# Kernel tuning notes

Measured on AMD Instinct MI355X. Metric: run time of the kernel, lower is better.

Reference implementation:

```python
import jax, jax.numpy as jnp
import numpy as np

NUM_HEADS = 16


def setup_inputs() -> dict:
    k0 = jax.random.key(0)
    ks = jax.random.split(k0, 5)
    T, S, N, E = 1024, 1024, 8, 1024
    query = jax.random.normal(ks[0], (T, N, E), dtype=jnp.float32)
    key_t = jax.random.normal(ks[1], (S, N, E), dtype=jnp.float32)
    value = jax.random.normal(ks[2], (S, N, E), dtype=jnp.float32)
    # xavier-uniform-like scale for in_proj (fan_in=fan_out-ish): gain*sqrt(6/(3E+E))
    lim_in = float(np.sqrt(6.0 / (3 * E + E)))
    in_proj_weight = jax.random.uniform(ks[3], (3 * E, E), dtype=jnp.float32, minval=-lim_in, maxval=lim_in)
    in_proj_bias = jnp.zeros((3 * E,), dtype=jnp.float32)
    lim_out = float(np.sqrt(1.0 / E))
    out_proj_weight = jax.random.uniform(ks[4], (E, E), dtype=jnp.float32, minval=-lim_out, maxval=lim_out)
    out_proj_bias = jnp.zeros((E,), dtype=jnp.float32)
    return {
        'query': query, 'key': key_t, 'value': value,
        'in_proj_weight': in_proj_weight, 'in_proj_bias': in_proj_bias,
        'out_proj_weight': out_proj_weight, 'out_proj_bias': out_proj_bias,
    }


def reference(query, key, value, in_proj_weight, in_proj_bias, out_proj_weight, out_proj_bias):
    # Faithful to the source: q,k,v ALL come from `query` via the 3E in-projection
    # (the torch code projects only `query` and chunks; key/value tensors unused).
    T, N, E = query.shape
    S = key.shape[0]  # must equal T for the reshape, as in the torch code
    H = NUM_HEADS
    D = E // H
    qkv = jnp.einsum('tne,fe->tnf', query, in_proj_weight) + in_proj_bias  # (T,N,3E)
    q, k, v = jnp.split(qkv, 3, axis=-1)
    q = q * (float(D) ** -0.5)
    # (T, N*H, D) -> (N*H, T, D)
    q = q.reshape(T, N * H, D).transpose(1, 0, 2)
    k = k.reshape(S, N * H, D).transpose(1, 0, 2)
    v = v.reshape(S, N * H, D).transpose(1, 0, 2)
    attn = jnp.einsum('btd,bsd->bts', q, k)          # (N*H, T, S)
    attn = jax.nn.softmax(attn, axis=-1)
    out = jnp.einsum('bts,bsd->btd', attn, v)        # (N*H, T, D)
    out = out.transpose(1, 0, 2).reshape(T, N, E)
    out = jnp.einsum('tne,fe->tnf', out, out_proj_weight) + out_proj_bias
    avg_weights = attn.reshape(N, H, T, S).mean(axis=1)  # (N, T, S)
    return out, avg_weights
```

## Files before the change

kernel.cpp:

```cpp
#include <hip/hip_runtime.h>


typedef __bf16 bf16x8 __attribute__((ext_vector_type(8)));
typedef float f32x4 __attribute__((ext_vector_type(4)));
typedef unsigned int u32;
typedef const __attribute__((address_space(1))) u32 gu32;
typedef __attribute__((address_space(3))) u32 lu32;

#define MFMA(a, b, c) __builtin_amdgcn_mfma_f32_16x16x32_bf16((a), (b), (c), 0, 0, 0)

#if __has_builtin(__builtin_amdgcn_exp2f)
#define EXP2(x) __builtin_amdgcn_exp2f(x)
#else
#define EXP2(x) exp2f(x)
#endif

__device__ __forceinline__ unsigned short f2bf(float x) {
    union { float f; unsigned u; } v; v.f = x;
    unsigned r = v.u + 0x7fffu + ((v.u >> 16) & 1u);
    return (unsigned short)(r >> 16);
}

__device__ __forceinline__ bf16x8 frag_ld(const unsigned short* p) {
    return __builtin_bit_cast(bf16x8, *(const uint4*)p);
}

template<int ROWS>
__device__ __forceinline__ void stageNx64(const unsigned short* g, int gs,
                                          unsigned short* lds, int wave, int lane) {
#pragma unroll
    for (int it = 0; it < ROWS / 32; it++) {
        int chunk = wave * (ROWS / 32) + it;
        int row = chunk * 8 + (lane >> 3);
        int cb = (lane & 7) ^ (row & 7);
        const unsigned short* gp = g + (size_t)row * gs + cb * 8;
        unsigned short* lp = lds + chunk * 512;
        __builtin_amdgcn_global_load_lds((gu32*)gp, (lu32*)lp, 16, 0, 0);
    }
}

__device__ __forceinline__ bf16x8 frag_sw(const unsigned short* lds, int row, int cb) {
    return frag_ld(lds + row * 64 + ((cb ^ (row & 7)) << 3));
}

__global__ void k_convert_all(const float* __restrict__ q, const float* __restrict__ wi,
                              const float* __restrict__ wo,
                              unsigned short* __restrict__ xq, unsigned short* __restrict__ xwi,
                              unsigned short* __restrict__ xwo) {
    int i = blockIdx.x * 256 + threadIdx.x;
    const float* src; unsigned short* dst; int off;
    if (i < 2097152)      { src = q;  dst = xq;  off = i; }
    else if (i < 2883584) { src = wi; dst = xwi; off = i - 2097152; }
    else                  { src = wo; dst = xwo; off = i - 2883584; }
    float4 v = ((const float4*)src)[off];
    ushort4 o;
    o.x = f2bf(v.x); o.y = f2bf(v.y); o.z = f2bf(v.z); o.w = f2bf(v.w);
    ((ushort4*)dst)[off] = o;
}

__global__ __launch_bounds__(256) void k_inproj(
    const unsigned short* __restrict__ A, const unsigned short* __restrict__ B,
    const float* __restrict__ bias,
    unsigned short* __restrict__ qbf, unsigned short* __restrict__ kbf,
    unsigned short* __restrict__ vTbf)
{
    __shared__ unsigned short As[2][128 * 64];
    __shared__ unsigned short Bs[2][128 * 64];
    const int tid = threadIdx.x;
    const int wave = tid >> 6, lane = tid & 63;
    const int quad = lane >> 4, l16 = lane & 15;
    const int wm = wave >> 1, wn = wave & 1;
    const int m0 = blockIdx.x * 128, n0 = blockIdx.y * 128;
    const unsigned short* Ab = A + (size_t)m0 * 1024;
    const unsigned short* Bb = B + (size_t)n0 * 1024;

    f32x4 acc[4][4];
#pragma unroll
    for (int i = 0; i < 4; i++)
#pragma unroll
        for (int j = 0; j < 4; j++) acc[i][j] = (f32x4){0.f, 0.f, 0.f, 0.f};

    stageNx64<128>(Ab, 1024, As[0], wave, lane);
    stageNx64<128>(Bb, 1024, Bs[0], wave, lane);
    __syncthreads();
    for (int it = 0; it < 16; it++) {
        const int cur = it & 1;
        if (it < 15) {
            stageNx64<128>(Ab + (it + 1) * 64, 1024, As[cur ^ 1], wave, lane);
            stageNx64<128>(Bb + (it + 1) * 64, 1024, Bs[cur ^ 1], wave, lane);
        }
#pragma unroll
        for (int kc = 0; kc < 2; kc++) {
            bf16x8 af[4], bfr[4];
#pragma unroll
            for (int i = 0; i < 4; i++) af[i]  = frag_sw(As[cur], wm * 64 + i * 16 + l16, kc * 4 + quad);
#pragma unroll
            for (int j = 0; j < 4; j++) bfr[j] = frag_sw(Bs[cur], wn * 64 + j * 16 + l16, kc * 4 + quad);
#pragma unroll
            for (int i = 0; i < 4; i++)
#pragma unroll
                for (int j = 0; j < 4; j++) acc[i][j] = MFMA(af[i], bfr[j], acc[i][j]);
        }
        __syncthreads();
    }
    const float QSCALE = 0.125f * 1.4426950408889634f;
    const int c = n0 >> 10;
#pragma unroll
    for (int i = 0; i < 4; i++) {
#pragma unroll
        for (int j = 0; j < 4; j++) {
            int col = n0 + wn * 64 + j * 16 + l16;
            float bv = bias[col];
            int hd = col & 1023;
#pragma unroll
            for (int r = 0; r < 4; r++) {
                int row = m0 + wm * 64 + i * 16 + quad * 4 + r;
                float val = acc[i][j][r] + bv;
                if (c == 0)      qbf[(size_t)row * 1024 + hd] = f2bf(val * QSCALE);
                else if (c == 1) kbf[(size_t)row * 1024 + hd] = f2bf(val);
                else {
                    int h = hd >> 6, d = hd & 63;
                    int t = row >> 3, n = row & 7;
                    int b = n * 16 + h;
                    vTbf[(size_t)b * 65536 + (size_t)d * 1024 + t] = f2bf(val);
                }
            }
        }
    }
}

__global__ __launch_bounds__(256) void k_pv(
    const unsigned short* __restrict__ qbf, const unsigned short* __restrict__ kbf,
    const unsigned short* __restrict__ vTbf,
    float* __restrict__ il_g, unsigned short* __restrict__ Obf)
{
    __shared__ unsigned short Ks[2][64 * 64];
    __shared__ unsigned short Vs[2][64 * 64];
    __shared__ unsigned short Ps[128 * 64];
    const int tid = threadIdx.x;
    const int wave = tid >> 6, lane = tid & 63, quad = lane >> 4, l16 = lane & 15;
    const int blk = blockIdx.x;
    const int xcd = blk & 7, idx = blk >> 3;
    const int b = xcd * 16 + (idx >> 3);
    const int t0 = (idx & 7) * 128;
    const int n = b >> 4, h = b & 15;
    const size_t vb = (size_t)b * 65536;
    const size_t qkb = (size_t)n * 1024 + h * 64;

    bf16x8 aq[2][2];
#pragma unroll
    for (int rf = 0; rf < 2; rf++)
#pragma unroll
        for (int kh = 0; kh < 2; kh++)
            aq[rf][kh] = frag_ld(&qbf[(size_t)(t0 + wave * 32 + rf * 16 + l16) * 8192 + qkb + kh * 32 + quad * 8]);

    float lsum[2][4];
    f32x4 o[2][4];
#pragma unroll
    for (int rf = 0; rf < 2; rf++)
#pragma unroll
        for (int r = 0; r < 4; r++) lsum[rf][r] = 0.f;
#pragma unroll
    for (int rf = 0; rf < 2; rf++)
#pragma unroll
        for (int df = 0; df < 4; df++) o[rf][df] = (f32x4){0.f, 0.f, 0.f, 0.f};

    stageNx64<64>(kbf + qkb, 8192, Ks[0], wave, lane);
    stageNx64<64>(vTbf + vb, 1024, Vs[0], wave, lane);
    __syncthreads();
    for (int st = 0; st < 16; st++) {
        const int cur = st & 1;
        if (st < 15) {
            stageNx64<64>(kbf + qkb + (size_t)(st + 1) * 524288, 8192, Ks[cur ^ 1], wave, lane);
            stageNx64<64>(vTbf + vb + (st + 1) * 64, 1024, Vs[cur ^ 1], wave, lane);
        }
#pragma unroll
        for (int cf = 0; cf < 4; cf++) {
            bf16x8 k0 = frag_sw(Ks[cur], cf * 16 + l16, quad);
            bf16x8 k1 = frag_sw(Ks[cur], cf * 16 + l16, 4 + quad);
#pragma unroll
            for (int rf = 0; rf < 2; rf++) {
                f32x4 z = (f32x4){0.f, 0.f, 0.f, 0.f};
                z = MFMA(aq[rf][0], k0, z);
                z = MFMA(aq[rf][1], k1, z);
#pragma unroll
                for (int r = 0; r < 4; r++) {
                    float p = EXP2(z[r]);
                    lsum[rf][r] += p;
                    int prow = wave * 32 + rf * 16 + quad * 4 + r;
                    int col = cf * 16 + l16;
                    Ps[prow * 64 + (((col >> 3) ^ (prow & 7)) << 3) + (col & 7)] = f2bf(p);
                }
            }
        }
#pragma unroll
        for (int kc = 0; kc < 2; kc++) {
            bf16x8 ap0 = frag_sw(Ps, wave * 32 + l16, kc * 4 + quad);
            bf16x8 ap1 = frag_sw(Ps, wave * 32 + 16 + l16, kc * 4 + quad);
#pragma unroll
            for (int df = 0; df < 4; df++) {
                bf16x8 bv = frag_sw(Vs[cur], df * 16 + l16, kc * 4 + quad);
                o[0][df] = MFMA(ap0, bv, o[0][df]);
                o[1][df] = MFMA(ap1, bv, o[1][df]);
            }
        }
        __syncthreads();
    }
#pragma unroll
    for (int rf = 0; rf < 2; rf++)
#pragma unroll
        for (int r = 0; r < 4; r++) {
            float s = lsum[rf][r];
            s += __shfl_xor(s, 1); s += __shfl_xor(s, 2);
            s += __shfl_xor(s, 4); s += __shfl_xor(s, 8);
            lsum[rf][r] = 1.0f / s;
        }
#pragma unroll
    for (int rf = 0; rf < 2; rf++)
#pragma unroll
        for (int df = 0; df < 4; df++)
#pragma unroll
            for (int r = 0; r < 4; r++) {
                int t = t0 + wave * 32 + rf * 16 + quad * 4 + r;
                Obf[(size_t)(t * 8 + n) * 1024 + h * 64 + df * 16 + l16] = f2bf(o[rf][df][r] * lsum[rf][r]);
            }
    if (l16 == 0) {
#pragma unroll
        for (int rf = 0; rf < 2; rf++)
#pragma unroll
            for (int r = 0; r < 4; r++)
                il_g[(size_t)b * 1024 + t0 + wave * 32 + rf * 16 + quad * 4 + r] = lsum[rf][r];
    }
}

__global__ __launch_bounds__(256) void k_avg(
    const unsigned short* __restrict__ qbf, const unsigned short* __restrict__ kbf,
    const float* __restrict__ il_g, float* __restrict__ avg)
{
    __shared__ unsigned short Qs[2][128 * 64];
    __shared__ unsigned short Ks[2][128 * 64];
    __shared__ float Is[16 * 128];
    const int tid = threadIdx.x;
    const int wave = tid >> 6, lane = tid & 63, quad = lane >> 4, l16 = lane & 15;
    const int wm = wave >> 1, wn = wave & 1;
    const int blk = blockIdx.x;
    const int n = blk & 7, idx = blk >> 3;
    const int s0 = (idx & 7) * 128, t0 = (idx >> 3) * 128;

    for (int i2 = tid; i2 < 2048; i2 += 256)
        Is[i2] = il_g[(size_t)(n * 16 + (i2 >> 7)) * 1024 + t0 + (i2 & 127)];

    f32x4 acc[4][4];
#pragma unroll
    for (int i = 0; i < 4; i++)
#pragma unroll
        for (int j = 0; j < 4; j++) acc[i][j] = (f32x4){0.f, 0.f, 0.f, 0.f};

    const size_t qb = (size_t)t0 * 8192 + (size_t)n * 1024;
    const size_t kb = (size_t)s0 * 8192 + (size_t)n * 1024;
    stageNx64<128>(qbf + qb, 8192, Qs[0], wave, lane);
    stageNx64<128>(kbf + kb, 8192, Ks[0], wave, lane);
    __syncthreads();
    for (int h = 0; h < 16; h++) {
        const int cur = h & 1;
        if (h < 15) {
            stageNx64<128>(qbf + qb + (h + 1) * 64, 8192, Qs[cur ^ 1], wave, lane);
            stageNx64<128>(kbf + kb + (h + 1) * 64, 8192, Ks[cur ^ 1], wave, lane);
        }
        bf16x8 af[4][2];
        float ir[4][4];
#pragma unroll
        for (int i = 0; i < 4; i++) {
            af[i][0] = frag_sw(Qs[cur], wm * 64 + i * 16 + l16, quad);
            af[i][1] = frag_sw(Qs[cur], wm * 64 + i * 16 + l16, 4 + quad);
#pragma unroll
            for (int r = 0; r < 4; r++) ir[i][r] = Is[h * 128 + wm * 64 + i * 16 + quad * 4 + r];
        }
#pragma unroll
        for (int j = 0; j < 4; j++) {
            bf16x8 b0 = frag_sw(Ks[cur], wn * 64 + j * 16 + l16, quad);
            bf16x8 b1 = frag_sw(Ks[cur], wn * 64 + j * 16 + l16, 4 + quad);
#pragma unroll
            for (int i = 0; i < 4; i++) {
                f32x4 z = (f32x4){0.f, 0.f, 0.f, 0.f};
                z = MFMA(af[i][0], b0, z);
                z = MFMA(af[i][1], b1, z);
#pragma unroll
                for (int r = 0; r < 4; r++)
                    acc[i][j][r] += EXP2(z[r]) * ir[i][r];
            }
        }
        __syncthreads();
    }
#pragma unroll
    for (int i = 0; i < 4; i++)
#pragma unroll
        for (int j = 0; j < 4; j++)
#pragma unroll
            for (int r = 0; r < 4; r++) {
                int t = t0 + wm * 64 + i * 16 + quad * 4 + r;
                int s = s0 + wn * 64 + j * 16 + l16;
                avg[(size_t)n * 1048576 + (size_t)t * 1024 + s] = acc[i][j][r] * 0.0625f;
            }
}

__global__ __launch_bounds__(256) void k_outproj(
    const unsigned short* __restrict__ A, const unsigned short* __restrict__ B,
    const float* __restrict__ bias, float* __restrict__ out)
{
    __shared__ unsigned short As[2][128 * 64];
    __shared__ unsigned short Bs[2][128 * 64];
    const int tid = threadIdx.x;
    const int wave = tid >> 6, lane = tid & 63;
    const int quad = lane >> 4, l16 = lane & 15;
    const int wm = wave >> 1, wn = wave & 1;
    const int m0 = blockIdx.x * 128, n0 = blockIdx.y * 128;
    const unsigned short* Ab = A + (size_t)m0 * 1024;
    const unsigned short* Bb = B + (size_t)n0 * 1024;

    f32x4 acc[4][4];
#pragma unroll
    for (int i = 0; i < 4; i++)
#pragma unroll
        for (int j = 0; j < 4; j++) acc[i][j] = (f32x4){0.f, 0.f, 0.f, 0.f};

    stageNx64<128>(Ab, 1024, As[0], wave, lane);
    stageNx64<128>(Bb, 1024, Bs[0], wave, lane);
    __syncthreads();
    for (int it = 0; it < 16; it++) {
        const int cur = it & 1;
        if (it < 15) {
            stageNx64<128>(Ab + (it + 1) * 64, 1024, As[cur ^ 1], wave, lane);
            stageNx64<128>(Bb + (it + 1) * 64, 1024, Bs[cur ^ 1], wave, lane);
        }
#pragma unroll
        for (int kc = 0; kc < 2; kc++) {
            bf16x8 af[4], bfr[4];
#pragma unroll
            for (int i = 0; i < 4; i++) af[i]  = frag_sw(As[cur], wm * 64 + i * 16 + l16, kc * 4 + quad);
#pragma unroll
            for (int j = 0; j < 4; j++) bfr[j] = frag_sw(Bs[cur], wn * 64 + j * 16 + l16, kc * 4 + quad);
#pragma unroll
            for (int i = 0; i < 4; i++)
#pragma unroll
                for (int j = 0; j < 4; j++) acc[i][j] = MFMA(af[i], bfr[j], acc[i][j]);
        }
        __syncthreads();
    }
#pragma unroll
    for (int i = 0; i < 4; i++)
#pragma unroll
        for (int j = 0; j < 4; j++) {
            int col = n0 + wn * 64 + j * 16 + l16;
            float bv = bias[col];
#pragma unroll
            for (int r = 0; r < 4; r++) {
                int row = m0 + wm * 64 + i * 16 + quad * 4 + r;
                out[(size_t)row * 1024 + col] = acc[i][j][r] + bv;
            }
        }
}

extern "C" void kernel_launch(void* const* d_in, const int* in_sizes, int n_in,
                              void* d_out, int out_size, void* d_ws, size_t ws_size,
                              hipStream_t stream)
{
    const float* query = (const float*)d_in[0];
    const float* w_in  = (const float*)d_in[3];
    const float* b_in  = (const float*)d_in[4];
    const float* w_out = (const float*)d_in[5];
    const float* b_out = (const float*)d_in[6];
    float* out = (float*)d_out;
    float* avg = out + 8388608;

    if (ws_size < ((size_t)73 << 20)) return;

    char* ws = (char*)d_ws;
    unsigned short* qbf  = (unsigned short*)(ws);
    unsigned short* kbf  = (unsigned short*)(ws + ((size_t)16 << 20));
    unsigned short* vTbf = (unsigned short*)(ws + ((size_t)32 << 20));
    unsigned short* xbf  = (unsigned short*)(ws + ((size_t)48 << 20));
    unsigned short* wibf = (unsigned short*)(ws + ((size_t)64 << 20));
    unsigned short* wobf = (unsigned short*)(ws + ((size_t)70 << 20));
    float* il_g = (float*)(ws + ((size_t)72 << 20));

    k_convert_all<<<12288, 256, 0, stream>>>(query, w_in, w_out, xbf, wibf, wobf);
    k_inproj<<<dim3(64, 24), 256, 0, stream>>>(xbf, wibf, b_in, qbf, kbf, vTbf);
    k_pv    <<<1024, 256, 0, stream>>>(qbf, kbf, vTbf, il_g, xbf);
    k_avg   <<<512, 256, 0, stream>>>(qbf, kbf, il_g, avg);
    k_outproj<<<dim3(64, 8), 256, 0, stream>>>(xbf, wobf, b_out, out);
}
```

Before: 359.9 us.

## Merge avg-weights and out-projection into one launch; remap inproj block order

The avg-weights kernel and the out-projection GEMM are independent, so they now run as one launch: blocks 0-511 do the avg work and blocks 512-1023 do the out-projection, sharing one shared-memory buffer. This removes a kernel launch and the tail gap between them, and lets the two workloads overlap on the CUs. The in-projection kernel also permutes its M-block index so concurrently running blocks hit different rows, which may change L2 locality. The merged kernel's register use and shared memory are set by the larger of the two branches, which can reduce occupancy for the out-projection part.

```diff
diff --git a/kernel.cpp b/kernel.cpp
--- a/kernel.cpp
+++ b/kernel.cpp
@@ -70,7 +70,9 @@
     const int wave = tid >> 6, lane = tid & 63;
     const int quad = lane >> 4, l16 = lane & 15;
     const int wm = wave >> 1, wn = wave & 1;
-    const int m0 = blockIdx.x * 128, n0 = blockIdx.y * 128;
+    const int bx = blockIdx.x;
+    const int mx = (bx & 7) * 8 + (bx >> 3);
+    const int m0 = mx * 128, n0 = blockIdx.y * 128;
     const unsigned short* Ab = A + (size_t)m0 * 1024;
     const unsigned short* Bb = B + (size_t)n0 * 1024;
 
@@ -233,132 +235,130 @@
     }
 }
 
-__global__ __launch_bounds__(256) void k_avg(
+__global__ __launch_bounds__(256) void k_avg_outproj(
     const unsigned short* __restrict__ qbf, const unsigned short* __restrict__ kbf,
-    const float* __restrict__ il_g, float* __restrict__ avg)
+    const float* __restrict__ il_g, float* __restrict__ avg,
+    const unsigned short* __restrict__ A, const unsigned short* __restrict__ B,
+    const float* __restrict__ bias, float* __restrict__ out)
 {
-    __shared__ unsigned short Qs[2][128 * 64];
-    __shared__ unsigned short Ks[2][128 * 64];
-    __shared__ float Is[16 * 128];
+    __shared__ unsigned short smem[36864];
     const int tid = threadIdx.x;
     const int wave = tid >> 6, lane = tid & 63, quad = lane >> 4, l16 = lane & 15;
     const int wm = wave >> 1, wn = wave & 1;
-    const int blk = blockIdx.x;
-    const int n = blk & 7, idx = blk >> 3;
-    const int s0 = (idx & 7) * 128, t0 = (idx >> 3) * 128;
-
-    for (int i2 = tid; i2 < 2048; i2 += 256)
-        Is[i2] = il_g[(size_t)(n * 16 + (i2 >> 7)) * 1024 + t0 + (i2 & 127)];
-
-    f32x4 acc[4][4];
-#pragma unroll
-    for (int i = 0; i < 4; i++)
-#pragma unroll
-        for (int j = 0; j < 4; j++) acc[i][j] = (f32x4){0.f, 0.f, 0.f, 0.f};
-
-    const size_t qb = (size_t)t0 * 8192 + (size_t)n * 1024;
-    const size_t kb = (size_t)s0 * 8192 + (size_t)n * 1024;
-    stageNx64<128>(qbf + qb, 8192, Qs[0], wave, lane);
-    stageNx64<128>(kbf + kb, 8192, Ks[0], wave, lane);
-    __syncthreads();
-    for (int h = 0; h < 16; h++) {
-        const int cur = h & 1;
-        if (h < 15) {
-            stageNx64<128>(qbf + qb + (h + 1) * 64, 8192, Qs[cur ^ 1], wave, lane);
-            stageNx64<128>(kbf + kb + (h + 1) * 64, 8192, Ks[cur ^ 1], wave, lane);
-        }
-        bf16x8 af[4][2];
-        float ir[4][4];
-#pragma unroll
-        for (int i = 0; i < 4; i++) {
-            af[i][0] = frag_sw(Qs[cur], wm * 64 + i * 16 + l16, quad);
-            af[i][1] = frag_sw(Qs[cur], wm * 64 + i * 16 + l16, 4 + quad);
-#pragma unroll
-            for (int r = 0; r < 4; r++) ir[i][r] = Is[h * 128 + wm * 64 + i * 16 + quad * 4 + r];
-        }
-#pragma unroll
-        for (int j = 0; j < 4; j++) {
-            bf16x8 b0 = frag_sw(Ks[cur], wn * 64 + j * 16 + l16, quad);
-            bf16x8 b1 = frag_sw(Ks[cur], wn * 64 + j * 16 + l16, 4 + quad);
+
+    if (blockIdx.x < 512) {
+        unsigned short (*Qs)[128 * 64] = (unsigned short (*)[128 * 64])(smem);
+        unsigned short (*Ks)[128 * 64] = (unsigned short (*)[128 * 64])(smem + 16384);
+        float* Is = (float*)(smem + 32768);
+        const int blk = blockIdx.x;
+        const int n = blk & 7, idx = blk >> 3;
+        const int s0 = (idx & 7) * 128, t0 = (idx >> 3) * 128;
+
+        for (int i2 = tid; i2 < 2048; i2 += 256)
+            Is[i2] = il_g[(size_t)(n * 16 + (i2 >> 7)) * 1024 + t0 + (i2 & 127)];
+
+        f32x4 acc[4][4];
+#pragma unroll
+        for (int i = 0; i < 4; i++)
+#pragma unroll
+            for (int j = 0; j < 4; j++) acc[i][j] = (f32x4){0.f, 0.f, 0.f, 0.f};
+
+        const size_t qb = (size_t)t0 * 8192 + (size_t)n * 1024;
+        const size_t kb = (size_t)s0 * 8192 + (size_t)n * 1024;
+        stageNx64<128>(qbf + qb, 8192, Qs[0], wave, lane);
+        stageNx64<128>(kbf + kb, 8192, Ks[0], wave, lane);
+        __syncthreads();
+        for (int h = 0; h < 16; h++) {
+            const int cur = h & 1;
+            if (h < 15) {
+                stageNx64<128>(qbf + qb + (h + 1) * 64, 8192, Qs[cur ^ 1], wave, lane);
+                stageNx64<128>(kbf + kb + (h + 1) * 64, 8192, Ks[cur ^ 1], wave, lane);
+            }
+            bf16x8 af[4][2];
+            float ir[4][4];
 #pragma unroll
             for (int i = 0; i < 4; i++) {
-                f32x4 z = (f32x4){0.f, 0.f, 0.f, 0.f};
-                z = MFMA(af[i][0], b0, z);
-                z = MFMA(af[i][1], b1, z);
-#pragma unroll
-                for (int r = 0; r < 4; r++)
-                    acc[i][j][r] += EXP2(z[r]) * ir[i][r];
-            }
-        }
+                af[i][0] = frag_sw(Qs[cur], wm * 64 + i * 16 + l16, quad);
+                af[i][1] = frag_sw(Qs[cur], wm * 64 + i * 16 + l16, 4 + quad);
+#pragma unroll
+                for (int r = 0; r < 4; r++) ir[i][r] = Is[h * 128 + wm * 64 + i * 16 + quad * 4 + r];
+            }
+#pragma unroll
+            for (int j = 0; j < 4; j++) {
+                bf16x8 b0 = frag_sw(Ks[cur], wn * 64 + j * 16 + l16, quad);
+                bf16x8 b1 = frag_sw(Ks[cur], wn * 64 + j * 16 + l16, 4 + quad);
+#pragma unroll
+                for (int i = 0; i < 4; i++) {
+                    f32x4 z = (f32x4){0.f, 0.f, 0.f, 0.f};
+                    z = MFMA(af[i][0], b0, z);
+                    z = MFMA(af[i][1], b1, z);
+#pragma unroll
+                    for (int r = 0; r < 4; r++)
+                        acc[i][j][r] += EXP2(z[r]) * ir[i][r];
+                }
+            }
+            __syncthreads();
+        }
+#pragma unroll
+        for (int i = 0; i < 4; i++)
+#pragma unroll
+            for (int j = 0; j < 4; j++)
+#pragma unroll
+                for (int r = 0; r < 4; r++) {
+                    int t = t0 + wm * 64 + i * 16 + quad * 4 + r;
+                    int s = s0 + wn * 64 + j * 16 + l16;
+                    avg[(size_t)n * 1048576 + (size_t)t * 1024 + s] = acc[i][j][r] * 0.0625f;
+                }
+    } else {
+        unsigned short (*As)[128 * 64] = (unsigned short (*)[128 * 64])(smem);
+        unsigned short (*Bs)[128 * 64] = (unsigned short (*)[128 * 64])(smem + 16384);
+        const int ob = blockIdx.x - 512;
+        const int m0 = (ob & 63) * 128, n0 = (ob >> 6) * 128;
+        const unsigned short* Ab = A + (size_t)m0 * 1024;
+        const unsigned short* Bb = B + (size_t)n0 * 1024;
+
+        f32x4 acc[4][4];
+#pragma unroll
+        for (int i = 0; i < 4; i++)
+#pragma unroll
+            for (int j = 0; j < 4; j++) acc[i][j] = (f32x4){0.f, 0.f, 0.f, 0.f};
+
+        stageNx64<128>(Ab, 1024, As[0], wave, lane);
+        stageNx64<128>(Bb, 1024, Bs[0], wave, lane);
         __syncthreads();
-    }
-#pragma unroll
-    for (int i = 0; i < 4; i++)
-#pragma unroll
-        for (int j = 0; j < 4; j++)
-#pragma unroll
-            for (int r = 0; r < 4; r++) {
-                int t = t0 + wm * 64 + i * 16 + quad * 4 + r;
-                int s = s0 + wn * 64 + j * 16 + l16;
-                avg[(size_t)n * 1048576 + (size_t)t * 1024 + s] = acc[i][j][r] * 0.0625f;
-            }
-}
-
-__global__ __launch_bounds__(256) void k_outproj(
-    const unsigned short* __restrict__ A, const unsigned short* __restrict__ B,
-    const float* __restrict__ bias, float* __restrict__ out)
-{
-    __shared__ unsigned short As[2][128 * 64];
-    __shared__ unsigned short Bs[2][128 * 64];
-    const int tid = threadIdx.x;
-    const int wave = tid >> 6, lane = tid & 63;
-    const int quad = lane >> 4, l16 = lane & 15;
-    const int wm = wave >> 1, wn = wave & 1;
-    const int m0 = blockIdx.x * 128, n0 = blockIdx.y * 128;
-    const unsigned short* Ab = A + (size_t)m0 * 1024;
-    const unsigned short* Bb = B + (size_t)n0 * 1024;
-
-    f32x4 acc[4][4];
-#pragma unroll
-    for (int i = 0; i < 4; i++)
-#pragma unroll
-        for (int j = 0; j < 4; j++) acc[i][j] = (f32x4){0.f, 0.f, 0.f, 0.f};
-
-    stageNx64<128>(Ab, 1024, As[0], wave, lane);
-    stageNx64<128>(Bb, 1024, Bs[0], wave, lane);
-    __syncthreads();
-    for (int it = 0; it < 16; it++) {
-        const int cur = it & 1;
-        if (it < 15) {
-            stageNx64<128>(Ab + (it + 1) * 64, 1024, As[cur ^ 1], wave, lane);
-            stageNx64<128>(Bb + (it + 1) * 64, 1024, Bs[cur ^ 1], wave, lane);
-        }
-#pragma unroll
-        for (int kc = 0; kc < 2; kc++) {
-            bf16x8 af[4], bfr[4];
-#pragma unroll
-            for (int i = 0; i < 4; i++) af[i]  = frag_sw(As[cur], wm * 64 + i * 16 + l16, kc * 4 + quad);
-#pragma unroll
-            for (int j = 0; j < 4; j++) bfr[j] = frag_sw(Bs[cur], wn * 64 + j * 16 + l16, kc * 4 + quad);
-#pragma unroll
-            for (int i = 0; i < 4; i++)
-#pragma unroll
-                for (int j = 0; j < 4; j++) acc[i][j] = MFMA(af[i], bfr[j], acc[i][j]);
-        }
-        __syncthreads();
-    }
-#pragma unroll
-    for (int i = 0; i < 4; i++)
-#pragma unroll
-        for (int j = 0; j < 4; j++) {
-            int col = n0 + wn * 64 + j * 16 + l16;
-            float bv = bias[col];
-#pragma unroll
-            for (int r = 0; r < 4; r++) {
-                int row = m0 + wm * 64 + i * 16 + quad * 4 + r;
-                out[(size_t)row * 1024 + col] = acc[i][j][r] + bv;
-            }
-        }
+        for (int it = 0; it < 16; it++) {
+            const int cur = it & 1;
+            if (it < 15) {
+                stageNx64<128>(Ab + (it + 1) * 64, 1024, As[cur ^ 1], wave, lane);
+                stageNx64<128>(Bb + (it + 1) * 64, 1024, Bs[cur ^ 1], wave, lane);
+            }
+#pragma unroll
+            for (int kc = 0; kc < 2; kc++) {
+                bf16x8 af[4], bfr[4];
+#pragma unroll
+                for (int i = 0; i < 4; i++) af[i]  = frag_sw(As[cur], wm * 64 + i * 16 + l16, kc * 4 + quad);
+#pragma unroll
+                for (int j = 0; j < 4; j++) bfr[j] = frag_sw(Bs[cur], wn * 64 + j * 16 + l16, kc * 4 + quad);
+#pragma unroll
+                for (int i = 0; i < 4; i++)
+#pragma unroll
+                    for (int j = 0; j < 4; j++) acc[i][j] = MFMA(af[i], bfr[j], acc[i][j]);
+            }
+            __syncthreads();
+        }
+#pragma unroll
+        for (int i = 0; i < 4; i++)
+#pragma unroll
+            for (int j = 0; j < 4; j++) {
+                int col = n0 + wn * 64 + j * 16 + l16;
+                float bv = bias[col];
+#pragma unroll
+                for (int r = 0; r < 4; r++) {
+                    int row = m0 + wm * 64 + i * 16 + quad * 4 + r;
+                    out[(size_t)row * 1024 + col] = acc[i][j][r] + bv;
+                }
+            }
+    }
 }
 
 extern "C" void kernel_launch(void* const* d_in, const int* in_sizes, int n_in,
@@ -387,6 +387,5 @@
     k_convert_all<<<12288, 256, 0, stream>>>(query, w_in, w_out, xbf, wibf, wobf);
     k_inproj<<<dim3(64, 24), 256, 0, stream>>>(xbf, wibf, b_in, qbf, kbf, vTbf);
     k_pv    <<<1024, 256, 0, stream>>>(qbf, kbf, vTbf, il_g, xbf);
-    k_avg   <<<512, 256, 0, stream>>>(qbf, kbf, il_g, avg);
-    k_outproj<<<dim3(64, 8), 256, 0, stream>>>(xbf, wobf, b_out, out);
-}
+    k_avg_outproj<<<1024, 256, 0, stream>>>(qbf, kbf, il_g, avg, xbf, wobf, b_out, out);
+}
```

Result: no change. 357.3 us (-0.7%).
